# Kernel tuning notes

Measured on AMD Instinct MI355X. Metric: run time of the kernel, lower is better.

The kernel has to match this reference:

```python
import jax, jax.numpy as jnp
import numpy as np

N_NODE = 100000
EMB = 128
N_EDGES = 1600000
LAYERS = 2
EPS = 1e-12  # torch F.normalize default eps


def setup_inputs() -> dict:
    key = jax.random.key(0)
    k1, k2, k3, k4, k5, k6 = jax.random.split(key, 6)
    return {
        "user_emb_weight": jax.random.normal(k1, (N_NODE, EMB), jnp.float32) * 0.02,
        "gate_w": jax.random.normal(k2, (EMB, EMB), jnp.float32) * (1.0 / np.sqrt(EMB)),
        "gate_b": jax.random.normal(k3, (EMB,), jnp.float32) * 0.01,
        "edge_rows": jax.random.randint(k4, (N_EDGES,), 0, N_NODE, jnp.int32),
        "edge_cols": jax.random.randint(k5, (N_EDGES,), 0, N_NODE, jnp.int32),
        "edge_vals": jax.random.uniform(k6, (N_EDGES,), jnp.float32),
        "layers": LAYERS,
    }


def _spmm(rows, cols, vals, x, n):
    # sparse [n,n] @ dense [n,d]: out[r] += v * x[c]
    gathered = vals[:, None] * x[cols]          # [nnz, d]
    return jax.ops.segment_sum(gathered, rows, num_segments=n)


def _l2_normalize(x):
    norm = jnp.sqrt(jnp.sum(x * x, axis=1, keepdims=True))
    return x / jnp.maximum(norm, EPS)


def reference(user_emb_weight, gate_w, gate_b, edge_rows, edge_cols, edge_vals, layers):
    n = user_emb_weight.shape[0]
    # self_gating: em * sigmoid(em @ W + b)
    u = user_emb_weight * jax.nn.sigmoid(user_emb_weight @ gate_w + gate_b)
    acc = u
    for _ in range(layers):
        u = _spmm(edge_rows, edge_cols, edge_vals, u, n)
        acc = acc + _l2_normalize(u)
    return acc
```

## Files before the change

### kernel.cpp

```cpp
#include <hip/hip_runtime.h>


typedef short s16x8 __attribute__((ext_vector_type(8)));
typedef float f32x4 __attribute__((ext_vector_type(4)));

__device__ __forceinline__ float bflo(unsigned u) {
    union { unsigned u; float f; } x; x.u = u << 16; return x.f;
}
__device__ __forceinline__ float bfhi(unsigned u) {
    union { unsigned u; float f; } x; x.u = u & 0xffff0000u; return x.f;
}
__device__ __forceinline__ float bf1(unsigned short s) {
    union { unsigned u; float f; } x; x.u = (unsigned)s << 16; return x.f;
}
__device__ __forceinline__ unsigned short f2bf(float f) {
    union { float f; unsigned u; } x; x.f = f;
    unsigned r = x.u + 0x7fffu + ((x.u >> 16) & 1u);
    return (unsigned short)(r >> 16);
}
__device__ __forceinline__ unsigned pack2(float a, float b) {
    return (unsigned)f2bf(a) | ((unsigned)f2bf(b) << 16);
}
__device__ __forceinline__ float i2f(int i) {
    union { int i; float f; } x; x.i = i; return x.f;
}
__device__ __forceinline__ int f2i(float f) {
    union { float f; int i; } x; x.f = f; return x.i;
}

__global__ void detect_kernel(const unsigned* __restrict__ em, int nwords,
                              int* __restrict__ mode) {
    __shared__ int bad_s;
    if (threadIdx.x == 0) bad_s = 0;
    __syncthreads();
    int bad = 0;
    for (int i = threadIdx.x; i < nwords; i += blockDim.x) {
        unsigned u = em[i];
        unsigned e0 = (u >> 7) & 0xFFu;
        unsigned e1 = (u >> 23) & 0xFFu;
        if (e0 >= 157u || e1 >= 157u) bad = 1;
    }
    if (bad) atomicOr(&bad_s, 1);
    __syncthreads();
    if (threadIdx.x == 0) mode[0] = bad_s;
}

__global__ __launch_bounds__(256) void gating_mfma_kernel(
    const void* __restrict__ emv, const void* __restrict__ Wv,
    const void* __restrict__ bv,
    unsigned short* __restrict__ u_out,
    const int* __restrict__ mode_p, int n)
{
    __shared__ __align__(16) unsigned short Wt[128 * 136];
    const int fp32 = mode_p[0];
    const int tid = threadIdx.x;

    if (fp32) {
        const float* W = (const float*)Wv;
        for (int i = tid; i < 16384; i += 256) {
            int k = i >> 7, c = i & 127;
            Wt[c * 136 + k] = f2bf(W[i]);
        }
    } else {
        const unsigned short* W = (const unsigned short*)Wv;
        for (int i = tid; i < 16384; i += 256) {
            int k = i >> 7, c = i & 127;
            Wt[c * 136 + k] = W[i];
        }
    }
    __syncthreads();

    const int wave = tid >> 6, lane = tid & 63;
    const int quad = lane >> 4, l16 = lane & 15;

    s16x8 bfrag[8][4];
#pragma unroll
    for (int t = 0; t < 8; ++t)
#pragma unroll
        for (int kb = 0; kb < 4; ++kb) {
            int col = t * 16 + l16;
            int k = kb * 32 + quad * 8;
            bfrag[t][kb] = *(const s16x8*)&Wt[col * 136 + k];
        }

    float bias[8];
    if (fp32) {
        const float* b = (const float*)bv;
#pragma unroll
        for (int t = 0; t < 8; ++t) bias[t] = b[t * 16 + l16];
    } else {
        const unsigned short* b = (const unsigned short*)bv;
#pragma unroll
        for (int t = 0; t < 8; ++t) bias[t] = bf1(b[t * 16 + l16]);
    }

    const int nstrips = (n + 15) >> 4;
    const int gwaves = gridDim.x * 4;
    for (int s = blockIdx.x * 4 + wave; s < nstrips; s += gwaves) {
        const int m0 = s * 16;
        const int arow = m0 + l16;

        s16x8 afrag[4];
        if (fp32) {
            const float* em = (const float*)emv;
#pragma unroll
            for (int kb = 0; kb < 4; ++kb) {
                union { unsigned u[4]; s16x8 v; } cv;
                if (arow < n) {
                    const float* src = em + (size_t)arow * 128 + kb * 32 + quad * 8;
                    float4 f0 = *(const float4*)(src);
                    float4 f1 = *(const float4*)(src + 4);
                    cv.u[0] = pack2(f0.x, f0.y); cv.u[1] = pack2(f0.z, f0.w);
                    cv.u[2] = pack2(f1.x, f1.y); cv.u[3] = pack2(f1.z, f1.w);
                } else { cv.u[0] = cv.u[1] = cv.u[2] = cv.u[3] = 0; }
                afrag[kb] = cv.v;
            }
        } else {
            const unsigned short* em = (const unsigned short*)emv;
#pragma unroll
            for (int kb = 0; kb < 4; ++kb) {
                union { uint4 u; s16x8 v; } cv;
                if (arow < n)
                    cv.u = *(const uint4*)(em + (size_t)arow * 128 + kb * 32 + quad * 8);
                else
                    cv.u = make_uint4(0, 0, 0, 0);
                afrag[kb] = cv.v;
            }
        }

        f32x4 acc[8];
#pragma unroll
        for (int t = 0; t < 8; ++t) {
            f32x4 a = {0.f, 0.f, 0.f, 0.f};
#pragma unroll
            for (int kb = 0; kb < 4; ++kb)
                a = __builtin_amdgcn_mfma_f32_16x16x32_bf16(afrag[kb], bfrag[t][kb], a, 0, 0, 0);
            acc[t] = a;
        }

#pragma unroll
        for (int t = 0; t < 8; ++t) {
            const int col = t * 16 + l16;
#pragma unroll
            for (int r = 0; r < 4; ++r) {
                const int row = m0 + quad * 4 + r;
                if (row < n) {
                    float e;
                    if (fp32) e = ((const float*)emv)[(size_t)row * 128 + col];
                    else      e = bf1(((const unsigned short*)emv)[(size_t)row * 128 + col]);
                    float g = 1.f / (1.f + __expf(-(acc[t][r] + bias[t])));
                    u_out[(size_t)row * 128 + col] = f2bf(e * g);
                }
            }
        }
    }
}

#define CHUNK 4096
#define MAXE  5120

__global__ __launch_bounds__(256) void bucket_hist_kernel(
    const int* __restrict__ erow, int* __restrict__ bcnt, int nnz)
{
    __shared__ int l[512];
    int tid = threadIdx.x;
    l[tid] = 0; l[tid + 256] = 0;
    __syncthreads();
    int c0 = blockIdx.x * CHUNK;
    int cend = min(c0 + CHUNK, nnz);
    for (int i = c0 + tid; i < cend; i += 256)
        atomicAdd(&l[(unsigned)erow[i] >> 8], 1);
    __syncthreads();
    if (l[tid]) atomicAdd(&bcnt[tid], l[tid]);
    if (l[tid + 256]) atomicAdd(&bcnt[tid + 256], l[tid + 256]);
}

__global__ __launch_bounds__(256) void bucket_scan_kernel(
    const int* __restrict__ bcnt, int* __restrict__ bbase,
    int* __restrict__ gcursor, int* __restrict__ rp, int n, int B, int nnz)
{
    __shared__ int s[512], tsum[256];
    int tid = threadIdx.x;
    s[tid] = (tid < B) ? bcnt[tid] : 0;
    s[tid + 256] = (tid + 256 < B) ? bcnt[tid + 256] : 0;
    __syncthreads();
    int a0 = s[2 * tid], a1 = s[2 * tid + 1];
    tsum[tid] = a0 + a1;
    __syncthreads();
#pragma unroll
    for (int off = 1; off < 256; off <<= 1) {
        int t = (tid >= off) ? tsum[tid - off] : 0;
        __syncthreads();
        tsum[tid] += t;
        __syncthreads();
    }
    int excl = (tid == 0) ? 0 : tsum[tid - 1];
    if (2 * tid < B)     { bbase[2 * tid] = excl;          gcursor[2 * tid] = excl; }
    if (2 * tid + 1 < B) { bbase[2 * tid + 1] = excl + a0; gcursor[2 * tid + 1] = excl + a0; }
    if (tid == 0) { bbase[B] = nnz; rp[n] = nnz; }
}

__global__ __launch_bounds__(256) void partition_kernel(
    const int* __restrict__ erow, const int* __restrict__ ecol,
    const void* __restrict__ eval, int* __restrict__ gcursor,
    int2* __restrict__ sev_tmp, const int* __restrict__ mode_p, int nnz)
{
    __shared__ int lcnt[512], lbase[512];
    int tid = threadIdx.x;
    lcnt[tid] = 0; lcnt[tid + 256] = 0;
    __syncthreads();
    int c0 = blockIdx.x * CHUNK;
    int cend = min(c0 + CHUNK, nnz);
    for (int i = c0 + tid; i < cend; i += 256)
        atomicAdd(&lcnt[(unsigned)erow[i] >> 8], 1);
    __syncthreads();
    int c256 = lcnt[tid], c512 = lcnt[tid + 256];
    if (c256 > 0) lbase[tid] = atomicAdd(&gcursor[tid], c256);
    if (c512 > 0) lbase[tid + 256] = atomicAdd(&gcursor[tid + 256], c512);
    __syncthreads();
    lcnt[tid] = 0; lcnt[tid + 256] = 0;
    __syncthreads();
    const int fp32 = mode_p[0];
    for (int i = c0 + tid; i < cend; i += 256) {
        int row = erow[i];
        int bkt = (unsigned)row >> 8;
        int rank = atomicAdd(&lcnt[bkt], 1);
        float v = fp32 ? ((const float*)eval)[i]
                       : bf1(((const unsigned short*)eval)[i]);
        int x = ((row & 255) << 17) | ecol[i];
        sev_tmp[lbase[bkt] + rank] = make_int2(x, f2i(v));
    }
}

__global__ __launch_bounds__(256) void csr_fin_kernel(
    const int* __restrict__ bbase, const int2* __restrict__ sev_tmp,
    int2* __restrict__ sev, int* __restrict__ rp, int n)
{
    __shared__ int2 ev[MAXE];
    __shared__ int rcnt[256], tsum[256];
    int b = blockIdx.x;
    int base = bbase[b];
    int size = bbase[b + 1] - base;
    int tid = threadIdx.x;
    rcnt[tid] = 0;
    __syncthreads();
    bool fits = (size <= MAXE);
    if (fits) {
        for (int e = tid; e < size; e += 256) {
            int2 t = sev_tmp[base + e];
            ev[e] = t;
            atomicAdd(&rcnt[(unsigned)t.x >> 17], 1);
        }
    } else {
        for (int e = tid; e < size; e += 256)
            atomicAdd(&rcnt[(unsigned)sev_tmp[base + e].x >> 17], 1);
    }
    __syncthreads();
    int myc = rcnt[tid];
    tsum[tid] = myc;
    __syncthreads();
#pragma unroll
    for (int off = 1; off < 256; off <<= 1) {
        int t = (tid >= off) ? tsum[tid - off] : 0;
        __syncthreads();
        tsum[tid] += t;
        __syncthreads();
    }
    int excl = tsum[tid] - myc;
    int row0 = b << 8;
    if (row0 + tid < n) rp[row0 + tid] = base + excl;
    __syncthreads();
    rcnt[tid] = excl;
    __syncthreads();
    for (int e = tid; e < size; e += 256) {
        int2 t = fits ? ev[e] : sev_tmp[base + e];
        int r = (unsigned)t.x >> 17;
        int k = atomicAdd(&rcnt[r], 1);
        sev[base + k] = make_int2(t.x & 0x1FFFF, t.y);
    }
}

__global__ __launch_bounds__(256) void spmm_norm_kernel(
    const int* __restrict__ rp, const int2* __restrict__ sev,
    const uint4* __restrict__ u_in, uint4* __restrict__ u_out,
    float* __restrict__ scale_out,
    const uint4* __restrict__ g_in, const uint4* __restrict__ prev_u,
    const float* __restrict__ prev_scale,
    void* __restrict__ out, const int* __restrict__ mode_p, int n)
{
    int w = (int)((blockIdx.x * (unsigned)blockDim.x + threadIdx.x) >> 6);
    int lane = threadIdx.x & 63;
    if (w >= n) return;
    const int q = lane >> 4, l16 = lane & 15;
    int e0 = rp[w], e1 = rp[w + 1];
    float a[8] = {0, 0, 0, 0, 0, 0, 0, 0};

    if (e1 > e0) {
        int e = e0;
        for (; e + 8 <= e1; e += 8) {
            int2 m0 = sev[e + q];
            int2 m1 = sev[e + 4 + q];
            uint4 g0 = u_in[(size_t)m0.x * 16 + l16];
            uint4 g1 = u_in[(size_t)m1.x * 16 + l16];
            float v0 = i2f(m0.y), v1 = i2f(m1.y);
            a[0] = fmaf(v0, bflo(g0.x), a[0]); a[1] = fmaf(v0, bfhi(g0.x), a[1]);
            a[2] = fmaf(v0, bflo(g0.y), a[2]); a[3] = fmaf(v0, bfhi(g0.y), a[3]);
            a[4] = fmaf(v0, bflo(g0.z), a[4]); a[5] = fmaf(v0, bfhi(g0.z), a[5]);
            a[6] = fmaf(v0, bflo(g0.w), a[6]); a[7] = fmaf(v0, bfhi(g0.w), a[7]);
            a[0] = fmaf(v1, bflo(g1.x), a[0]); a[1] = fmaf(v1, bfhi(g1.x), a[1]);
            a[2] = fmaf(v1, bflo(g1.y), a[2]); a[3] = fmaf(v1, bfhi(g1.y), a[3]);
            a[4] = fmaf(v1, bflo(g1.z), a[4]); a[5] = fmaf(v1, bfhi(g1.z), a[5]);
            a[6] = fmaf(v1, bflo(g1.w), a[6]); a[7] = fmaf(v1, bfhi(g1.w), a[7]);
        }
        for (; e < e1; e += 4) {
            int idx = e + q;
            int safe = min(idx, e1 - 1);
            int2 m = sev[safe];
            float v = (idx < e1) ? i2f(m.y) : 0.f;
            uint4 g = u_in[(size_t)m.x * 16 + l16];
            a[0] = fmaf(v, bflo(g.x), a[0]); a[1] = fmaf(v, bfhi(g.x), a[1]);
            a[2] = fmaf(v, bflo(g.y), a[2]); a[3] = fmaf(v, bfhi(g.y), a[3]);
            a[4] = fmaf(v, bflo(g.z), a[4]); a[5] = fmaf(v, bfhi(g.z), a[5]);
            a[6] = fmaf(v, bflo(g.w), a[6]); a[7] = fmaf(v, bfhi(g.w), a[7]);
        }
    }

#pragma unroll
    for (int j = 0; j < 8; ++j) {
        a[j] += __shfl_xor(a[j], 16, 64);
        a[j] += __shfl_xor(a[j], 32, 64);
    }
    float s = 0.f;
#pragma unroll
    for (int j = 0; j < 8; ++j) s = fmaf(a[j], a[j], s);
#pragma unroll
    for (int off = 8; off > 0; off >>= 1) s += __shfl_xor(s, off, 64);
    float scale = 1.f / fmaxf(sqrtf(s), 1e-12f);

    if (q == 0 && u_out) {
        uint4 o;
        o.x = pack2(a[0], a[1]); o.y = pack2(a[2], a[3]);
        o.z = pack2(a[4], a[5]); o.w = pack2(a[6], a[7]);
        u_out[(size_t)w * 16 + l16] = o;
    }
    if (lane == 0 && scale_out) scale_out[w] = scale;

    if (q == 1 && prev_u) {
        float s1 = prev_scale[w];
        uint4 gv = g_in[(size_t)w * 16 + l16];
        uint4 p1 = prev_u[(size_t)w * 16 + l16];
        float r0 = bflo(gv.x) + bflo(p1.x) * s1 + a[0] * scale;
        float r1 = bfhi(gv.x) + bfhi(p1.x) * s1 + a[1] * scale;
        float r2 = bflo(gv.y) + bflo(p1.y) * s1 + a[2] * scale;
        float r3 = bfhi(gv.y) + bfhi(p1.y) * s1 + a[3] * scale;
        float r4 = bflo(gv.z) + bflo(p1.z) * s1 + a[4] * scale;
        float r5 = bfhi(gv.z) + bfhi(p1.z) * s1 + a[5] * scale;
        float r6 = bflo(gv.w) + bflo(p1.w) * s1 + a[6] * scale;
        float r7 = bfhi(gv.w) + bfhi(p1.w) * s1 + a[7] * scale;
        if (mode_p[0]) {
            float* ap = (float*)out + (size_t)w * 128 + l16 * 8;
            float4 c0, c1;
            c0.x = r0; c0.y = r1; c0.z = r2; c0.w = r3;
            c1.x = r4; c1.y = r5; c1.z = r6; c1.w = r7;
            *(float4*)ap = c0; *(float4*)(ap + 4) = c1;
        } else {
            uint4 o;
            o.x = pack2(r0, r1); o.y = pack2(r2, r3);
            o.z = pack2(r4, r5); o.w = pack2(r6, r7);
            ((uint4*)out)[(size_t)w * 16 + l16] = o;
        }
    }
}

extern "C" void kernel_launch(void* const* d_in, const int* in_sizes, int n_in,
                              void* d_out, int out_size, void* d_ws, size_t ws_size,
                              hipStream_t stream)
{
    const void* em   = d_in[0];
    const void* gw   = d_in[1];
    const void* gb   = d_in[2];
    const int*  erow = (const int*)d_in[3];
    const int*  ecol = (const int*)d_in[4];
    const void* eval = d_in[5];

    int n   = in_sizes[0] / 128;
    int nnz = in_sizes[3];
    int B   = (n + 255) >> 8;
    int nblk_e = (nnz + CHUNK - 1) / CHUNK;

    char* ws = (char*)d_ws;
    size_t off = 0;
    auto carve = [&](size_t bytes) -> void* {
        void* p = ws + off;
        off += (bytes + 255) & ~(size_t)255;
        return p;
    };
    size_t nd = (size_t)n * 128;
    int*      mode    = (int*)carve(4);
    unsigned* uA      = (unsigned*)carve(nd * 2);
    unsigned* uB      = (unsigned*)carve(nd * 2);
    int*      rp      = (int*)carve((size_t)(n + 1) * 4);
    float*    scale1  = (float*)carve((size_t)n * 4);
    int*      bcnt    = (int*)carve(512 * 4);
    int*      bbase   = (int*)carve(516 * 4);
    int*      gcursor = (int*)carve(512 * 4);
    int2*     sev     = (int2*)carve((size_t)nnz * 8);
    int2*     sev_tmp = (int2*)uB;

    hipMemsetAsync(bcnt, 0, 512 * 4, stream);
    detect_kernel<<<1, 256, 0, stream>>>((const unsigned*)em, 8192, mode);

    gating_mfma_kernel<<<512, 256, 0, stream>>>(em, gw, gb, (unsigned short*)uA, mode, n);
    bucket_hist_kernel<<<nblk_e, 256, 0, stream>>>(erow, bcnt, nnz);
    bucket_scan_kernel<<<1, 256, 0, stream>>>(bcnt, bbase, gcursor, rp, n, B, nnz);
    partition_kernel<<<nblk_e, 256, 0, stream>>>(erow, ecol, eval, gcursor, sev_tmp, mode, nnz);
    csr_fin_kernel<<<B, 256, 0, stream>>>(bbase, sev_tmp, sev, rp, n);

    spmm_norm_kernel<<<(n + 3) / 4, 256, 0, stream>>>(
        rp, sev, (const uint4*)uA, (uint4*)uB, scale1,
        nullptr, nullptr, nullptr, nullptr, mode, n);
    spmm_norm_kernel<<<(n + 3) / 4, 256, 0, stream>>>(
        rp, sev, (const uint4*)uB, nullptr, nullptr,
        (const uint4*)uA, (const uint4*)uB, scale1, d_out, mode, n);
}
```

Before: 363.7 us.

## Replace bucketed CSR build with per-row histogram, two-pass scan, and atomic scatter

The two-level bucket partition plus per-bucket finalize pass is replaced by a direct per-row global atomic histogram, a two-kernel prefix scan and an atomic-cursor scatter into CSR. Format detection is folded into the histogram launch as an extra block. The SpMM accumulation also switches to packed two-wide float FMA vectors. This drops one full pass over the edge list and the intermediate buffer, at the cost of heavy contention on global atomics and scattered 8-byte writes.

```diff
diff --git a/kernel.cpp b/kernel.cpp
--- a/kernel.cpp
+++ b/kernel.cpp
@@ -3,6 +3,7 @@
 
 typedef short s16x8 __attribute__((ext_vector_type(8)));
 typedef float f32x4 __attribute__((ext_vector_type(4)));
+typedef float f32x2 __attribute__((ext_vector_type(2)));
 
 __device__ __forceinline__ float bflo(unsigned u) {
     union { unsigned u; float f; } x; x.u = u << 16; return x.f;
@@ -27,22 +28,109 @@
 __device__ __forceinline__ int f2i(float f) {
     union { float f; int i; } x; x.f = f; return x.i;
 }
-
-__global__ void detect_kernel(const unsigned* __restrict__ em, int nwords,
-                              int* __restrict__ mode) {
-    __shared__ int bad_s;
-    if (threadIdx.x == 0) bad_s = 0;
+__device__ __forceinline__ f32x2 unpk(unsigned u) {
+    union { unsigned u; float f; } lo, hi;
+    lo.u = u << 16; hi.u = u & 0xffff0000u;
+    f32x2 p; p.x = lo.f; p.y = hi.f; return p;
+}
+
+#define CHUNK 4096
+#define SCANB 1024
+
+__global__ __launch_bounds__(256) void hist_detect_kernel(
+    const int* __restrict__ erow, int* __restrict__ cnt,
+    const unsigned* __restrict__ em, int* __restrict__ mode,
+    int nnz, int nblk)
+{
+    if ((int)blockIdx.x == nblk) {
+        __shared__ int bad_s;
+        if (threadIdx.x == 0) bad_s = 0;
+        __syncthreads();
+        int bad = 0;
+        for (int i = threadIdx.x; i < 8192; i += 256) {
+            unsigned u = em[i];
+            unsigned e0 = (u >> 7) & 0xFFu;
+            unsigned e1 = (u >> 23) & 0xFFu;
+            if (e0 >= 157u || e1 >= 157u) bad = 1;
+        }
+        if (bad) atomicOr(&bad_s, 1);
+        __syncthreads();
+        if (threadIdx.x == 0) mode[0] = bad_s;
+        return;
+    }
+    int c0 = blockIdx.x * CHUNK;
+    int cend = min(c0 + CHUNK, nnz);
+    for (int i = c0 + threadIdx.x; i < cend; i += 256)
+        atomicAdd(&cnt[erow[i]], 1);
+}
+
+__global__ __launch_bounds__(256) void scan1_kernel(
+    const int* __restrict__ cnt, int* __restrict__ rp,
+    int* __restrict__ bsum, int n)
+{
+    __shared__ int tsum[256];
+    const int tid = threadIdx.x;
+    const int r0 = blockIdx.x * SCANB + tid * 4;
+    int c[4];
+#pragma unroll
+    for (int j = 0; j < 4; ++j) c[j] = (r0 + j < n) ? cnt[r0 + j] : 0;
+    int T = c[0] + c[1] + c[2] + c[3];
+    tsum[tid] = T;
     __syncthreads();
-    int bad = 0;
-    for (int i = threadIdx.x; i < nwords; i += blockDim.x) {
-        unsigned u = em[i];
-        unsigned e0 = (u >> 7) & 0xFFu;
-        unsigned e1 = (u >> 23) & 0xFFu;
-        if (e0 >= 157u || e1 >= 157u) bad = 1;
-    }
-    if (bad) atomicOr(&bad_s, 1);
+#pragma unroll
+    for (int off = 1; off < 256; off <<= 1) {
+        int t = (tid >= off) ? tsum[tid - off] : 0;
+        __syncthreads();
+        tsum[tid] += t;
+        __syncthreads();
+    }
+    int s = tsum[tid] - T;
+#pragma unroll
+    for (int j = 0; j < 4; ++j) {
+        if (r0 + j < n) rp[r0 + j] = s;
+        s += c[j];
+    }
+    if (tid == 255) bsum[blockIdx.x] = tsum[255];
+}
+
+__global__ __launch_bounds__(256) void scan2_kernel(
+    int* __restrict__ rp, int* __restrict__ cursor,
+    const int* __restrict__ bsum, int n, int nnz, int nscan)
+{
+    __shared__ int red[256];
+    const int tid = threadIdx.x, b = blockIdx.x;
+    red[tid] = (tid < b) ? bsum[tid] : 0;
     __syncthreads();
-    if (threadIdx.x == 0) mode[0] = bad_s;
+#pragma unroll
+    for (int off = 128; off > 0; off >>= 1) {
+        if (tid < off) red[tid] += red[tid + off];
+        __syncthreads();
+    }
+    const int off0 = red[0];
+    const int r0 = b * SCANB + tid * 4;
+#pragma unroll
+    for (int j = 0; j < 4; ++j) {
+        int r = r0 + j;
+        if (r < n) { int v = rp[r] + off0; rp[r] = v; cursor[r] = v; }
+    }
+    if (b == nscan - 1 && tid == 0) rp[n] = nnz;
+}
+
+__global__ __launch_bounds__(256) void scatter_kernel(
+    const int* __restrict__ erow, const int* __restrict__ ecol,
+    const void* __restrict__ eval, int* __restrict__ cursor,
+    int2* __restrict__ sev, const int* __restrict__ mode_p, int nnz)
+{
+    const int fp32 = mode_p[0];
+    int c0 = blockIdx.x * CHUNK;
+    int cend = min(c0 + CHUNK, nnz);
+    for (int i = c0 + threadIdx.x; i < cend; i += 256) {
+        int row = erow[i];
+        float v = fp32 ? ((const float*)eval)[i]
+                       : bf1(((const unsigned short*)eval)[i]);
+        int k = atomicAdd(&cursor[row], 1);
+        sev[k] = make_int2(ecol[i], f2i(v));
+    }
 }
 
 __global__ __launch_bounds__(256) void gating_mfma_kernel(
@@ -156,130 +244,6 @@
     }
 }
 
-#define CHUNK 4096
-#define MAXE  5120
-
-__global__ __launch_bounds__(256) void bucket_hist_kernel(
-    const int* __restrict__ erow, int* __restrict__ bcnt, int nnz)
-{
-    __shared__ int l[512];
-    int tid = threadIdx.x;
-    l[tid] = 0; l[tid + 256] = 0;
-    __syncthreads();
-    int c0 = blockIdx.x * CHUNK;
-    int cend = min(c0 + CHUNK, nnz);
-    for (int i = c0 + tid; i < cend; i += 256)
-        atomicAdd(&l[(unsigned)erow[i] >> 8], 1);
-    __syncthreads();
-    if (l[tid]) atomicAdd(&bcnt[tid], l[tid]);
-    if (l[tid + 256]) atomicAdd(&bcnt[tid + 256], l[tid + 256]);
-}
-
-__global__ __launch_bounds__(256) void bucket_scan_kernel(
-    const int* __restrict__ bcnt, int* __restrict__ bbase,
-    int* __restrict__ gcursor, int* __restrict__ rp, int n, int B, int nnz)
-{
-    __shared__ int s[512], tsum[256];
-    int tid = threadIdx.x;
-    s[tid] = (tid < B) ? bcnt[tid] : 0;
-    s[tid + 256] = (tid + 256 < B) ? bcnt[tid + 256] : 0;
-    __syncthreads();
-    int a0 = s[2 * tid], a1 = s[2 * tid + 1];
-    tsum[tid] = a0 + a1;
-    __syncthreads();
-#pragma unroll
-    for (int off = 1; off < 256; off <<= 1) {
-        int t = (tid >= off) ? tsum[tid - off] : 0;
-        __syncthreads();
-        tsum[tid] += t;
-        __syncthreads();
-    }
-    int excl = (tid == 0) ? 0 : tsum[tid - 1];
-    if (2 * tid < B)     { bbase[2 * tid] = excl;          gcursor[2 * tid] = excl; }
-    if (2 * tid + 1 < B) { bbase[2 * tid + 1] = excl + a0; gcursor[2 * tid + 1] = excl + a0; }
-    if (tid == 0) { bbase[B] = nnz; rp[n] = nnz; }
-}
-
-__global__ __launch_bounds__(256) void partition_kernel(
-    const int* __restrict__ erow, const int* __restrict__ ecol,
-    const void* __restrict__ eval, int* __restrict__ gcursor,
-    int2* __restrict__ sev_tmp, const int* __restrict__ mode_p, int nnz)
-{
-    __shared__ int lcnt[512], lbase[512];
-    int tid = threadIdx.x;
-    lcnt[tid] = 0; lcnt[tid + 256] = 0;
-    __syncthreads();
-    int c0 = blockIdx.x * CHUNK;
-    int cend = min(c0 + CHUNK, nnz);
-    for (int i = c0 + tid; i < cend; i += 256)
-        atomicAdd(&lcnt[(unsigned)erow[i] >> 8], 1);
-    __syncthreads();
-    int c256 = lcnt[tid], c512 = lcnt[tid + 256];
-    if (c256 > 0) lbase[tid] = atomicAdd(&gcursor[tid], c256);
-    if (c512 > 0) lbase[tid + 256] = atomicAdd(&gcursor[tid + 256], c512);
-    __syncthreads();
-    lcnt[tid] = 0; lcnt[tid + 256] = 0;
-    __syncthreads();
-    const int fp32 = mode_p[0];
-    for (int i = c0 + tid; i < cend; i += 256) {
-        int row = erow[i];
-        int bkt = (unsigned)row >> 8;
-        int rank = atomicAdd(&lcnt[bkt], 1);
-        float v = fp32 ? ((const float*)eval)[i]
-                       : bf1(((const unsigned short*)eval)[i]);
-        int x = ((row & 255) << 17) | ecol[i];
-        sev_tmp[lbase[bkt] + rank] = make_int2(x, f2i(v));
-    }
-}
-
-__global__ __launch_bounds__(256) void csr_fin_kernel(
-    const int* __restrict__ bbase, const int2* __restrict__ sev_tmp,
-    int2* __restrict__ sev, int* __restrict__ rp, int n)
-{
-    __shared__ int2 ev[MAXE];
-    __shared__ int rcnt[256], tsum[256];
-    int b = blockIdx.x;
-    int base = bbase[b];
-    int size = bbase[b + 1] - base;
-    int tid = threadIdx.x;
-    rcnt[tid] = 0;
-    __syncthreads();
-    bool fits = (size <= MAXE);
-    if (fits) {
-        for (int e = tid; e < size; e += 256) {
-            int2 t = sev_tmp[base + e];
-            ev[e] = t;
-            atomicAdd(&rcnt[(unsigned)t.x >> 17], 1);
-        }
-    } else {
-        for (int e = tid; e < size; e += 256)
-            atomicAdd(&rcnt[(unsigned)sev_tmp[base + e].x >> 17], 1);
-    }
-    __syncthreads();
-    int myc = rcnt[tid];
-    tsum[tid] = myc;
-    __syncthreads();
-#pragma unroll
-    for (int off = 1; off < 256; off <<= 1) {
-        int t = (tid >= off) ? tsum[tid - off] : 0;
-        __syncthreads();
-        tsum[tid] += t;
-        __syncthreads();
-    }
-    int excl = tsum[tid] - myc;
-    int row0 = b << 8;
-    if (row0 + tid < n) rp[row0 + tid] = base + excl;
-    __syncthreads();
-    rcnt[tid] = excl;
-    __syncthreads();
-    for (int e = tid; e < size; e += 256) {
-        int2 t = fits ? ev[e] : sev_tmp[base + e];
-        int r = (unsigned)t.x >> 17;
-        int k = atomicAdd(&rcnt[r], 1);
-        sev[base + k] = make_int2(t.x & 0x1FFFF, t.y);
-    }
-}
-
 __global__ __launch_bounds__(256) void spmm_norm_kernel(
     const int* __restrict__ rp, const int2* __restrict__ sev,
     const uint4* __restrict__ u_in, uint4* __restrict__ u_out,
@@ -293,7 +257,7 @@
     if (w >= n) return;
     const int q = lane >> 4, l16 = lane & 15;
     int e0 = rp[w], e1 = rp[w + 1];
-    float a[8] = {0, 0, 0, 0, 0, 0, 0, 0};
+    f32x2 a0 = {0.f, 0.f}, a1 = {0.f, 0.f}, a2 = {0.f, 0.f}, a3 = {0.f, 0.f};
 
     if (e1 > e0) {
         int e = e0;
@@ -302,15 +266,16 @@
             int2 m1 = sev[e + 4 + q];
             uint4 g0 = u_in[(size_t)m0.x * 16 + l16];
             uint4 g1 = u_in[(size_t)m1.x * 16 + l16];
-            float v0 = i2f(m0.y), v1 = i2f(m1.y);
-            a[0] = fmaf(v0, bflo(g0.x), a[0]); a[1] = fmaf(v0, bfhi(g0.x), a[1]);
-            a[2] = fmaf(v0, bflo(g0.y), a[2]); a[3] = fmaf(v0, bfhi(g0.y), a[3]);
-            a[4] = fmaf(v0, bflo(g0.z), a[4]); a[5] = fmaf(v0, bfhi(g0.z), a[5]);
-            a[6] = fmaf(v0, bflo(g0.w), a[6]); a[7] = fmaf(v0, bfhi(g0.w), a[7]);
-            a[0] = fmaf(v1, bflo(g1.x), a[0]); a[1] = fmaf(v1, bfhi(g1.x), a[1]);
-            a[2] = fmaf(v1, bflo(g1.y), a[2]); a[3] = fmaf(v1, bfhi(g1.y), a[3]);
-            a[4] = fmaf(v1, bflo(g1.z), a[4]); a[5] = fmaf(v1, bfhi(g1.z), a[5]);
-            a[6] = fmaf(v1, bflo(g1.w), a[6]); a[7] = fmaf(v1, bfhi(g1.w), a[7]);
+            f32x2 vv0 = {i2f(m0.y), i2f(m0.y)};
+            f32x2 vv1 = {i2f(m1.y), i2f(m1.y)};
+            a0 = __builtin_elementwise_fma(vv0, unpk(g0.x), a0);
+            a1 = __builtin_elementwise_fma(vv0, unpk(g0.y), a1);
+            a2 = __builtin_elementwise_fma(vv0, unpk(g0.z), a2);
+            a3 = __builtin_elementwise_fma(vv0, unpk(g0.w), a3);
+            a0 = __builtin_elementwise_fma(vv1, unpk(g1.x), a0);
+            a1 = __builtin_elementwise_fma(vv1, unpk(g1.y), a1);
+            a2 = __builtin_elementwise_fma(vv1, unpk(g1.z), a2);
+            a3 = __builtin_elementwise_fma(vv1, unpk(g1.w), a3);
         }
         for (; e < e1; e += 4) {
             int idx = e + q;
@@ -318,12 +283,15 @@
             int2 m = sev[safe];
             float v = (idx < e1) ? i2f(m.y) : 0.f;
             uint4 g = u_in[(size_t)m.x * 16 + l16];
-            a[0] = fmaf(v, bflo(g.x), a[0]); a[1] = fmaf(v, bfhi(g.x), a[1]);
-            a[2] = fmaf(v, bflo(g.y), a[2]); a[3] = fmaf(v, bfhi(g.y), a[3]);
-            a[4] = fmaf(v, bflo(g.z), a[4]); a[5] = fmaf(v, bfhi(g.z), a[5]);
-            a[6] = fmaf(v, bflo(g.w), a[6]); a[7] = fmaf(v, bfhi(g.w), a[7]);
-        }
-    }
+            f32x2 vv = {v, v};
+            a0 = __builtin_elementwise_fma(vv, unpk(g.x), a0);
+            a1 = __builtin_elementwise_fma(vv, unpk(g.y), a1);
+            a2 = __builtin_elementwise_fma(vv, unpk(g.z), a2);
+            a3 = __builtin_elementwise_fma(vv, unpk(g.w), a3);
+        }
+    }
+
+    float a[8] = {a0.x, a0.y, a1.x, a1.y, a2.x, a2.y, a3.x, a3.y};
 
 #pragma unroll
     for (int j = 0; j < 8; ++j) {
@@ -385,8 +353,8 @@
 
     int n   = in_sizes[0] / 128;
     int nnz = in_sizes[3];
-    int B   = (n + 255) >> 8;
     int nblk_e = (nnz + CHUNK - 1) / CHUNK;
+    int nscan  = (n + SCANB - 1) / SCANB;
 
     char* ws = (char*)d_ws;
     size_t off = 0;
@@ -401,20 +369,18 @@
     unsigned* uB      = (unsigned*)carve(nd * 2);
     int*      rp      = (int*)carve((size_t)(n + 1) * 4);
     float*    scale1  = (float*)carve((size_t)n * 4);
-    int*      bcnt    = (int*)carve(512 * 4);
-    int*      bbase   = (int*)carve(516 * 4);
-    int*      gcursor = (int*)carve(512 * 4);
+    int*      cnt     = (int*)carve((size_t)n * 4);
+    int*      cursor  = (int*)carve((size_t)n * 4);
+    int*      bsum    = (int*)carve(256 * 4);
     int2*     sev     = (int2*)carve((size_t)nnz * 8);
-    int2*     sev_tmp = (int2*)uB;
-
-    hipMemsetAsync(bcnt, 0, 512 * 4, stream);
-    detect_kernel<<<1, 256, 0, stream>>>((const unsigned*)em, 8192, mode);
-
+
+    hipMemsetAsync(cnt, 0, (size_t)n * 4, stream);
+    hist_detect_kernel<<<nblk_e + 1, 256, 0, stream>>>(
+        erow, cnt, (const unsigned*)em, mode, nnz, nblk_e);
     gating_mfma_kernel<<<512, 256, 0, stream>>>(em, gw, gb, (unsigned short*)uA, mode, n);
-    bucket_hist_kernel<<<nblk_e, 256, 0, stream>>>(erow, bcnt, nnz);
-    bucket_scan_kernel<<<1, 256, 0, stream>>>(bcnt, bbase, gcursor, rp, n, B, nnz);
-    partition_kernel<<<nblk_e, 256, 0, stream>>>(erow, ecol, eval, gcursor, sev_tmp, mode, nnz);
-    csr_fin_kernel<<<B, 256, 0, stream>>>(bbase, sev_tmp, sev, rp, n);
+    scan1_kernel<<<nscan, 256, 0, stream>>>(cnt, rp, bsum, n);
+    scan2_kernel<<<nscan, 256, 0, stream>>>(rp, cursor, bsum, n, nnz, nscan);
+    scatter_kernel<<<nblk_e, 256, 0, stream>>>(erow, ecol, eval, cursor, sev, mode, nnz);
 
     spmm_norm_kernel<<<(n + 3) / 4, 256, 0, stream>>>(
         rp, sev, (const uint4*)uA, (uint4*)uB, scale1,
```

New measurement: 469.8 us. 1.29x slower.
